# Performance work log

Hardware: AMD Instinct MI355X
Metric: run time of the kernel (lower is better)

## Reference

```python
import jax, jax.numpy as jnp
from jax import lax
import numpy as np

D_STATE = 16
D_CONV = 4
GROUPS = 4
TOKEN = 8


def group_norm(x, w, b, groups, eps=1e-5):
    # x: [B, C, H, W]; torch GroupNorm semantics
    B, C, H, W = x.shape
    xg = x.reshape(B, groups, C // groups, H, W)
    mu = xg.mean(axis=(2, 3, 4), keepdims=True)
    var = ((xg - mu) ** 2).mean(axis=(2, 3, 4), keepdims=True)
    xg = (xg - mu) / jnp.sqrt(var + eps)
    return xg.reshape(B, C, H, W) * w[None, :, None, None] + b[None, :, None, None]


def mamba_fwd(x, in_w, conv_w, conv_b, xproj_w, dt_w, dt_b, A_log, D, out_w):
    # x: [B, L, d_model]. Faithful mamba_ssm Mamba forward (no biases on in/out proj).
    Bsz, L, _ = x.shape
    d_inner = in_w.shape[0] // 2
    dt_rank = dt_w.shape[1]
    xz = x @ in_w.T                                   # [B, L, 2*d_inner]
    xi, z = jnp.split(xz, 2, axis=-1)
    # causal depthwise conv1d (kernel D_CONV) + SiLU
    xc = lax.conv_general_dilated(
        xi.transpose(0, 2, 1), conv_w, window_strides=(1,),
        padding=[(D_CONV - 1, 0)], dimension_numbers=("NCH", "OIH", "NCH"),
        feature_group_count=d_inner)
    xc = jax.nn.silu(xc + conv_b[None, :, None]).transpose(0, 2, 1)  # [B, L, d_inner]
    xdb = xc @ xproj_w.T                               # [B, L, dt_rank + 2*d_state]
    dt, Bm, Cm = jnp.split(xdb, [dt_rank, dt_rank + D_STATE], axis=-1)
    dt = jax.nn.softplus(dt @ dt_w.T + dt_b)           # [B, L, d_inner]
    A = -jnp.exp(A_log)                                # [d_inner, d_state]
    dA = jnp.exp(dt[..., None] * A)                    # [B, L, d_inner, d_state]
    dBx = dt[..., None] * Bm[:, :, None, :] * xc[..., None]

    def step(h, inp):
        dA_t, dBx_t, C_t = inp                         # [B,di,ds],[B,di,ds],[B,ds]
        h = dA_t * h + dBx_t
        y = jnp.einsum('bds,bs->bd', h, C_t)
        return h, y

    h0 = jnp.zeros((Bsz, d_inner, D_STATE), dtype=x.dtype)
    _, ys = lax.scan(step, h0, (dA.transpose(1, 0, 2, 3),
                                dBx.transpose(1, 0, 2, 3),
                                Cm.transpose(1, 0, 2)))
    y = ys.transpose(1, 0, 2) + xc * D                 # skip term D*x
    y = y * jax.nn.silu(z)
    return y @ out_w.T


def setup_inputs() -> dict:
    key = jax.random.key(0)
    ks = iter(jax.random.split(key, 48))

    def rn(shape, s=0.02):
        return jax.random.normal(next(ks), shape, dtype=jnp.float32) * s

    B, C, H, W = 4, 64, 64, 64
    inp = {"x": jax.random.normal(next(ks), (B, C, H, W), dtype=jnp.float32)}

    def mamba_params(prefix, d_model):
        d_inner = 2 * d_model
        dt_rank = -(-d_model // 16)
        inp[prefix + "_in_w"] = rn((2 * d_inner, d_model))
        inp[prefix + "_conv_w"] = rn((d_inner, 1, D_CONV))
        inp[prefix + "_conv_b"] = rn((d_inner,))
        inp[prefix + "_xproj_w"] = rn((dt_rank + 2 * D_STATE, d_inner))
        inp[prefix + "_dt_w"] = rn((d_inner, dt_rank))
        inp[prefix + "_dt_b"] = rn((d_inner,)) + 0.5
        inp[prefix + "_A_log"] = jnp.log(jnp.tile(jnp.arange(1, D_STATE + 1, dtype=jnp.float32), (d_inner, 1)))
        inp[prefix + "_D"] = jnp.ones((d_inner,), jnp.float32)
        inp[prefix + "_out_w"] = rn((d_model, d_inner))

    mamba_params("spa", C)
    mamba_params("spe", -(-C // TOKEN))  # group_channel_num = ceil(64/8) = 8
    inp["spa_gn_w"] = jnp.ones((C,), jnp.float32)
    inp["spa_gn_b"] = jnp.zeros((C,), jnp.float32)
    inp["spe_gn_w"] = jnp.ones((C,), jnp.float32)
    inp["spe_gn_b"] = jnp.zeros((C,), jnp.float32)
    inp["att_w"] = jnp.full((2,), 0.5, jnp.float32)
    return inp


def reference(x,
              spa_in_w, spa_conv_w, spa_conv_b, spa_xproj_w, spa_dt_w, spa_dt_b,
              spa_A_log, spa_D, spa_out_w,
              spe_in_w, spe_conv_w, spe_conv_b, spe_xproj_w, spe_dt_w, spe_dt_b,
              spe_A_log, spe_D, spe_out_w,
              spa_gn_w, spa_gn_b, spe_gn_w, spe_gn_b, att_w):
    B, C, H, W = x.shape
    gcn = -(-C // TOKEN)  # C == TOKEN*gcn here, so no padding path is taken

    # --- SpaMamba: flatten all pixels into one sequence [1, B*H*W, C] ---
    xs = x.transpose(0, 2, 3, 1).reshape(1, -1, C)
    ys = mamba_fwd(xs, spa_in_w, spa_conv_w, spa_conv_b, spa_xproj_w,
                   spa_dt_w, spa_dt_b, spa_A_log, spa_D, spa_out_w)
    ys = ys.reshape(B, H, W, C).transpose(0, 3, 1, 2)
    spa = jax.nn.silu(group_norm(ys, spa_gn_w, spa_gn_b, GROUPS)) + x

    # --- SpeMamba: per-pixel spectral tokens [B*H*W, TOKEN, gcn] ---
    xe = x.transpose(0, 2, 3, 1).reshape(B * H * W, TOKEN, gcn)
    ye = mamba_fwd(xe, spe_in_w, spe_conv_w, spe_conv_b, spe_xproj_w,
                   spe_dt_w, spe_dt_b, spe_A_log, spe_D, spe_out_w)
    ye = ye.reshape(B, H, W, C).transpose(0, 3, 1, 2)
    spe = x + jax.nn.silu(group_norm(ye, spe_gn_w, spe_gn_b, GROUPS))

    w = jax.nn.softmax(att_w)
    return spa * w[0] + spe * w[1] + x
```

## Files before the change

### kernel.cpp

```cpp
#include <hip/hip_runtime.h>

__device__ __forceinline__ float siluf(float x){ return x / (1.f + __expf(-x)); }
__device__ __forceinline__ float softplusf(float x){
    return fmaxf(x, 0.f) + __logf(1.f + __expf(-fabsf(x)));
}
#if __has_builtin(__builtin_amdgcn_exp2f)
__device__ __forceinline__ float fexp2(float x){ return __builtin_amdgcn_exp2f(x); }
#else
__device__ __forceinline__ float fexp2(float x){ return exp2f(x); }
#endif

__global__ void __launch_bounds__(256) k_xpose(const float* __restrict__ x, float* __restrict__ xs){
    __shared__ float t[64][65];
    int blk = blockIdx.x;
    int b = blk >> 6;
    int hw0 = (blk & 63) << 6;
    int tid = threadIdx.x;
    if (blk == 0 && tid < 192) xs[tid] = 0.f;
    const float* xb = x + b*262144 + hw0;
    #pragma unroll
    for (int it = 0; it < 16; ++it){
        int idx = it*256 + tid;
        t[idx>>6][idx&63] = xb[(idx>>6)*4096 + (idx&63)];
    }
    __syncthreads();
    float* xsb = xs + 192 + (size_t)(b*4096 + hw0)*64;
    #pragma unroll
    for (int it = 0; it < 16; ++it){
        int idx = it*256 + tid;
        xsb[(idx>>6)*64 + (idx&63)] = t[idx&63][idx>>6];
    }
}

__global__ void __launch_bounds__(256) k_inproj_conv(const float* __restrict__ xs,
        const float* __restrict__ in_w, const float* __restrict__ cw, const float* __restrict__ cb,
        float* __restrict__ xc, float* __restrict__ zb){
    int tid = threadIdx.x;
    int l0 = blockIdx.x * 8;
    float wr[64];
    const float4* w4 = (const float4*)(in_w + tid*64);
    #pragma unroll
    for (int k = 0; k < 16; ++k){
        float4 v = w4[k];
        wr[4*k]=v.x; wr[4*k+1]=v.y; wr[4*k+2]=v.z; wr[4*k+3]=v.w;
    }
    if (tid < 128){
        float acc[11];
        #pragma unroll
        for (int r = 0; r < 11; ++r) acc[r] = 0.f;
        const float4* xr = ((const float4*)xs) + (size_t)l0*16;
        #pragma unroll
        for (int k = 0; k < 16; ++k){
            #pragma unroll
            for (int r = 0; r < 11; ++r){
                float4 v = xr[r*16 + k];
                acc[r] = fmaf(v.x, wr[4*k],   acc[r]);
                acc[r] = fmaf(v.y, wr[4*k+1], acc[r]);
                acc[r] = fmaf(v.z, wr[4*k+2], acc[r]);
                acc[r] = fmaf(v.w, wr[4*k+3], acc[r]);
            }
        }
        float cw0 = cw[tid*4+0], cw1 = cw[tid*4+1], cw2 = cw[tid*4+2], cw3 = cw[tid*4+3];
        float cbd = cb[tid];
        #pragma unroll
        for (int r = 0; r < 8; ++r){
            float a = fmaf(cw0, acc[r],   cbd);
            a = fmaf(cw1, acc[r+1], a);
            a = fmaf(cw2, acc[r+2], a);
            a = fmaf(cw3, acc[r+3], a);
            xc[(size_t)(l0+r)*128 + tid] = siluf(a);
        }
    } else {
        float acc[8];
        #pragma unroll
        for (int r = 0; r < 8; ++r) acc[r] = 0.f;
        const float4* xr = ((const float4*)(xs + 192)) + (size_t)l0*16;
        #pragma unroll
        for (int k = 0; k < 16; ++k){
            #pragma unroll
            for (int r = 0; r < 8; ++r){
                float4 v = xr[r*16 + k];
                acc[r] = fmaf(v.x, wr[4*k],   acc[r]);
                acc[r] = fmaf(v.y, wr[4*k+1], acc[r]);
                acc[r] = fmaf(v.z, wr[4*k+2], acc[r]);
                acc[r] = fmaf(v.w, wr[4*k+3], acc[r]);
            }
        }
        int dz = tid - 128;
        #pragma unroll
        for (int r = 0; r < 8; ++r) zb[(size_t)(l0+r)*128 + dz] = acc[r];
    }
}

__global__ void __launch_bounds__(256) k_p1_spe(
        const float* __restrict__ xc, const float* __restrict__ xpw, const float* __restrict__ dtw,
        const float* __restrict__ dtb, const float* __restrict__ A_log,
        float* __restrict__ Pb, float* __restrict__ Qb,
        const float* __restrict__ x,
        const float* __restrict__ ein_w, const float* __restrict__ ecw, const float* __restrict__ ecb,
        const float* __restrict__ expw, const float* __restrict__ edtw, const float* __restrict__ edtb,
        const float* __restrict__ eA_log, const float* __restrict__ eDv, const float* __restrict__ eow,
        float* __restrict__ ye, float* __restrict__ sp)
{
    __shared__ float smem[9960];
    const int tid = threadIdx.x;
    if (blockIdx.x < 512){
        float* sxc = smem;
        float* sbm = smem + 4096;
        float* dtr = smem + 4608;
        const int ch = blockIdx.x;
        {
            const float4* src = (const float4*)(xc + (size_t)ch*4096);
            float4* dst = (float4*)sxc;
            #pragma unroll
            for (int u = 0; u < 4; ++u) dst[u*256 + tid] = src[u*256 + tid];
        }
        __syncthreads();
        {
            int j = tid & 63, tg = tid >> 6;
            if (j < 20){
                const float4* w4  = (const float4*)(xpw + j*128);
                const float4* xc4 = (const float4*)sxc + tg*256;
                float acc[8];
                #pragma unroll
                for (int r = 0; r < 8; ++r) acc[r] = 0.f;
                #pragma unroll 8
                for (int k = 0; k < 32; ++k){
                    float4 w = w4[k];
                    #pragma unroll
                    for (int r = 0; r < 8; ++r){
                        float4 v = xc4[r*32 + k];
                        acc[r] = fmaf(v.x, w.x, acc[r]);
                        acc[r] = fmaf(v.y, w.y, acc[r]);
                        acc[r] = fmaf(v.z, w.z, acc[r]);
                        acc[r] = fmaf(v.w, w.w, acc[r]);
                    }
                }
                if (j < 4){
                    #pragma unroll
                    for (int r = 0; r < 8; ++r) dtr[(tg*8+r)*4 + j] = acc[r];
                } else {
                    #pragma unroll
                    for (int r = 0; r < 8; ++r) sbm[(tg*8+r)*16 + (j-4)] = acc[r];
                }
            }
        }
        __syncthreads();
        const int d  = tid & 127;
        const int sh = tid >> 7;
        float A8[8];
        {
            const float4* al4 = (const float4*)(A_log + d*16 + sh*8);
            float4 v0 = al4[0], v1 = al4[1];
            A8[0]=-__expf(v0.x)*1.44269504f; A8[1]=-__expf(v0.y)*1.44269504f;
            A8[2]=-__expf(v0.z)*1.44269504f; A8[3]=-__expf(v0.w)*1.44269504f;
            A8[4]=-__expf(v1.x)*1.44269504f; A8[5]=-__expf(v1.y)*1.44269504f;
            A8[6]=-__expf(v1.z)*1.44269504f; A8[7]=-__expf(v1.w)*1.44269504f;
        }
        float4 dw = *(const float4*)(dtw + d*4);
        float dbd = dtb[d];
        float P[8], Q[8];
        #pragma unroll
        for (int s = 0; s < 8; ++s){ P[s] = 1.f; Q[s] = 0.f; }
        #pragma unroll 4
        for (int i = 0; i < 32; ++i){
            float4 dt4 = *(const float4*)(dtr + i*4);
            float dv = dbd;
            dv = fmaf(dt4.x, dw.x, dv);
            dv = fmaf(dt4.y, dw.y, dv);
            dv = fmaf(dt4.z, dw.z, dv);
            dv = fmaf(dt4.w, dw.w, dv);
            float dt = softplusf(dv);
            float db = dt * sxc[i*128 + d];
            const float4* bmr = (const float4*)(sbm + i*16 + sh*8);
            float4 b0 = bmr[0], b1 = bmr[1];
            float bv[8] = {b0.x,b0.y,b0.z,b0.w,b1.x,b1.y,b1.z,b1.w};
            #pragma unroll
            for (int s = 0; s < 8; ++s){
                float a = fexp2(dt*A8[s]);
                P[s] *= a;
                Q[s] = fmaf(a, Q[s], db*bv[s]);
            }
        }
        float* Pp = Pb + (size_t)ch*2048 + d*16 + sh*8;
        float* Qp = Qb + (size_t)ch*2048 + d*16 + sh*8;
        ((float4*)Pp)[0] = make_float4(P[0],P[1],P[2],P[3]);
        ((float4*)Pp)[1] = make_float4(P[4],P[5],P[6],P[7]);
        ((float4*)Qp)[0] = make_float4(Q[0],Q[1],Q[2],Q[3]);
        ((float4*)Qp)[1] = make_float4(Q[4],Q[5],Q[6],Q[7]);
    } else {
        float* xe  = smem;
        float* xcl = smem + 1088;
        float* bml = smem + 3264;
        float* cml = smem + 5440;
        float* dtl = smem + 7616;
        float* yl  = smem + 7752;
        float* spg = smem + 9928;
        const int pix = tid >> 4;
        const int d   = tid & 15;
        const int eb  = blockIdx.x - 512;
        const int p0  = eb * 16;
        const int b   = p0 >> 12;
        const int hw0 = p0 & 4095;

        const float* xb = x + b*262144 + hw0;
        #pragma unroll
        for (int it = 0; it < 4; ++it){
            int idx = it*256 + tid;
            xe[(idx>>4)*17 + (idx&15)] = xb[(idx>>4)*4096 + (idx&15)];
        }
        __syncthreads();

        float wi[8], wz[8];
        #pragma unroll
        for (int g = 0; g < 8; ++g){ wi[g] = ein_w[d*8+g]; wz[g] = ein_w[(16+d)*8+g]; }
        float xi[8], zz[8];
        #pragma unroll
        for (int t = 0; t < 8; ++t){
            float ai = 0.f, az = 0.f;
            #pragma unroll
            for (int g = 0; g < 8; ++g){
                float v = xe[(t*8+g)*17 + pix];
                ai = fmaf(v, wi[g], ai);
                az = fmaf(v, wz[g], az);
            }
            xi[t] = ai; zz[t] = az;
        }
        float c0 = ecw[d*4+0], c1 = ecw[d*4+1], c2 = ecw[d*4+2], c3 = ecw[d*4+3];
        float cbd = ecb[d];
        float xcr[8];
        #pragma unroll
        for (int t = 0; t < 8; ++t){
            float a = fmaf(c3, xi[t], cbd);
            if (t >= 1) a = fmaf(c2, xi[t-1], a);
            if (t >= 2) a = fmaf(c1, xi[t-2], a);
            if (t >= 3) a = fmaf(c0, xi[t-3], a);
            xcr[t] = siluf(a);
            xcl[(t*16+d)*17 + pix] = xcr[t];
        }
        __syncthreads();

        {
            const float* wr = expw + d*16;
            #pragma unroll
            for (int t = 0; t < 8; ++t){
                float acc = 0.f;
                #pragma unroll
                for (int k = 0; k < 16; ++k) acc = fmaf(xcl[(t*16+k)*17 + pix], wr[k], acc);
                if (d == 0) dtl[t*17 + pix] = acc;
                else bml[(t*16+d-1)*17 + pix] = acc;
            }
        }
        {
            const float* wr = expw + (17+d)*16;
            #pragma unroll
            for (int t = 0; t < 8; ++t){
                float acc = 0.f;
                #pragma unroll
                for (int k = 0; k < 16; ++k) acc = fmaf(xcl[(t*16+k)*17 + pix], wr[k], acc);
                cml[(t*16+d)*17 + pix] = acc;
            }
        }
        if (d == 15){
            const float* wr = expw + 16*16;
            #pragma unroll
            for (int t = 0; t < 8; ++t){
                float acc = 0.f;
                #pragma unroll
                for (int k = 0; k < 16; ++k) acc = fmaf(xcl[(t*16+k)*17 + pix], wr[k], acc);
                bml[(t*16+15)*17 + pix] = acc;
            }
        }
        __syncthreads();

        float A16[16];
        #pragma unroll
        for (int s = 0; s < 16; ++s) A16[s] = -__expf(eA_log[d*16+s]) * 1.44269504f;
        float dwd = edtw[d], dbd = edtb[d], Dd = eDv[d];
        float h[16];
        #pragma unroll
        for (int s = 0; s < 16; ++s) h[s] = 0.f;
        #pragma unroll
        for (int t = 0; t < 8; ++t){
            float dtd = softplusf(fmaf(dtl[t*17 + pix], dwd, dbd));
            float db = dtd * xcr[t];
            float yp = 0.f;
            #pragma unroll
            for (int s = 0; s < 16; ++s){
                float a = fexp2(dtd*A16[s]);
                h[s] = fmaf(a, h[s], db*bml[(t*16+s)*17 + pix]);
                yp = fmaf(h[s], cml[(t*16+s)*17 + pix], yp);
            }
            yl[(t*16+d)*17 + pix] = (yp + xcr[t]*Dd) * siluf(zz[t]);
        }
        __syncthreads();

        int t = d >> 1, m0 = (d & 1)*4;
        float acc[4];
        #pragma unroll
        for (int mm = 0; mm < 4; ++mm){
            const float* wr = eow + (m0+mm)*16;
            float a = 0.f;
            #pragma unroll
            for (int k = 0; k < 16; ++k) a = fmaf(yl[(t*16+k)*17 + pix], wr[k], a);
            acc[mm] = a;
        }
        float4 o; o.x=acc[0]; o.y=acc[1]; o.z=acc[2]; o.w=acc[3];
        *(float4*)(ye + (size_t)(p0+pix)*64 + t*8 + m0) = o;

        float s  = acc[0]+acc[1]+acc[2]+acc[3];
        float ss = acc[0]*acc[0]+acc[1]*acc[1]+acc[2]*acc[2]+acc[3]*acc[3];
        s += __shfl_xor(s,1);  ss += __shfl_xor(ss,1);
        s += __shfl_xor(s,2);  ss += __shfl_xor(ss,2);
        s += __shfl_xor(s,16); ss += __shfl_xor(ss,16);
        s += __shfl_xor(s,32); ss += __shfl_xor(ss,32);
        int lane = tid & 63, wv = tid >> 6;
        if ((lane & 51) == 0){ spg[0*16 + wv*4 + ((lane>>2)&3)] = s; spg[16 + wv*4 + ((lane>>2)&3)] = ss; }
        __syncthreads();
        if (tid < 4){
            int blk = eb & 255;
            float S  = spg[0*16+0*4+tid]+spg[0*16+1*4+tid]+spg[0*16+2*4+tid]+spg[0*16+3*4+tid];
            float SS = spg[16+0*4+tid]+spg[16+1*4+tid]+spg[16+2*4+tid]+spg[16+3*4+tid];
            float* dst = sp + (size_t)(((4 + b)*4 + tid)*512 + blk*2);
            dst[0] = S; dst[1] = SS;
        }
    }
}

__global__ void __launch_bounds__(256) k_scan_p2a(const float* __restrict__ Pb,
        const float* __restrict__ Qb, float* __restrict__ Ps, float* __restrict__ Qs){
    int g = blockIdx.x*256 + threadIdx.x;
    int sup = g >> 11;
    int lane = g & 2047;
    float P = 1.f, Q = 0.f;
    for (int i = 0; i < 32; i += 8){
        float p[8], q[8];
        #pragma unroll
        for (int u = 0; u < 8; ++u){
            p[u] = Pb[(size_t)(sup*32+i+u)*2048 + lane];
            q[u] = Qb[(size_t)(sup*32+i+u)*2048 + lane];
        }
        #pragma unroll
        for (int u = 0; u < 8; ++u){
            P = p[u]*P;
            Q = fmaf(p[u], Q, q[u]);
        }
    }
    Ps[g] = P; Qs[g] = Q;
}

__global__ void __launch_bounds__(256) k_scan_p2c(const float* __restrict__ Pb,
        const float* __restrict__ Qb, const float* __restrict__ Ps,
        const float* __restrict__ Qs, float* __restrict__ Hs){
    int g = blockIdx.x*256 + threadIdx.x;
    int sup = g >> 11;
    int lane = g & 2047;
    float h = 0.f;
    for (int u = 0; u < sup; ++u){
        float p = Ps[u*2048 + lane];
        float q = Qs[u*2048 + lane];
        h = fmaf(p, h, q);
    }
    for (int i = 0; i < 32; i += 8){
        float p[8], q[8];
        #pragma unroll
        for (int u = 0; u < 8; ++u){
            p[u] = Pb[(size_t)(sup*32+i+u)*2048 + lane];
            q[u] = Qb[(size_t)(sup*32+i+u)*2048 + lane];
        }
        #pragma unroll
        for (int u = 0; u < 8; ++u){
            Hs[(size_t)(sup*32+i+u)*2048 + lane] = h;
            h = fmaf(p[u], h, q[u]);
        }
    }
}

__global__ void __launch_bounds__(256) k_scan_p3(const float* __restrict__ xc,
        const float* __restrict__ zb, const float* __restrict__ xpw, const float* __restrict__ dtw,
        const float* __restrict__ dtb, const float* __restrict__ A_log, const float* __restrict__ Dv,
        const float* __restrict__ Hs, const float* __restrict__ ow,
        float* __restrict__ ys, float* __restrict__ sp){
    __shared__ float sxc[32*128];
    __shared__ float ypl[2][32*128];
    __shared__ float sbm[32*16];
    __shared__ float scm[32*16];
    __shared__ __align__(16) float dtr[32][4];
    __shared__ float pgs[2][2][4];
    const int tid = threadIdx.x;
    const int ch = blockIdx.x;
    {
        const float4* src = (const float4*)(xc + (size_t)ch*4096);
        float4* dst = (float4*)sxc;
        #pragma unroll
        for (int u = 0; u < 4; ++u) dst[u*256 + tid] = src[u*256 + tid];
    }
    __syncthreads();
    {
        int j = tid & 63, tg = tid >> 6;
        if (j < 36){
            const float4* w4  = (const float4*)(xpw + j*128);
            const float4* xc4 = (const float4*)sxc + tg*256;
            float acc[8];
            #pragma unroll
            for (int r = 0; r < 8; ++r) acc[r] = 0.f;
            #pragma unroll 8
            for (int k = 0; k < 32; ++k){
                float4 w = w4[k];
                #pragma unroll
                for (int r = 0; r < 8; ++r){
                    float4 v = xc4[r*32 + k];
                    acc[r] = fmaf(v.x, w.x, acc[r]);
                    acc[r] = fmaf(v.y, w.y, acc[r]);
                    acc[r] = fmaf(v.z, w.z, acc[r]);
                    acc[r] = fmaf(v.w, w.w, acc[r]);
                }
            }
            if (j < 4){
                #pragma unroll
                for (int r = 0; r < 8; ++r) dtr[tg*8+r][j] = acc[r];
            } else if (j < 20){
                #pragma unroll
                for (int r = 0; r < 8; ++r) sbm[(tg*8+r)*16 + (j-4)] = acc[r];
            } else {
                #pragma unroll
                for (int r = 0; r < 8; ++r) scm[(tg*8+r)*16 + (j-20)] = acc[r];
            }
        }
    }
    __syncthreads();
    const int d  = tid & 127;
    const int sh = tid >> 7;
    float A8[8], h[8];
    {
        const float4* al4 = (const float4*)(A_log + d*16 + sh*8);
        float4 v0 = al4[0], v1 = al4[1];
        A8[0]=-__expf(v0.x)*1.44269504f; A8[1]=-__expf(v0.y)*1.44269504f;
        A8[2]=-__expf(v0.z)*1.44269504f; A8[3]=-__expf(v0.w)*1.44269504f;
        A8[4]=-__expf(v1.x)*1.44269504f; A8[5]=-__expf(v1.y)*1.44269504f;
        A8[6]=-__expf(v1.z)*1.44269504f; A8[7]=-__expf(v1.w)*1.44269504f;
        const float4* h4 = (const float4*)(Hs + (size_t)ch*2048 + d*16 + sh*8);
        float4 h0 = h4[0], h1 = h4[1];
        h[0]=h0.x; h[1]=h0.y; h[2]=h0.z; h[3]=h0.w;
        h[4]=h1.x; h[5]=h1.y; h[6]=h1.z; h[7]=h1.w;
    }
    float4 dw = *(const float4*)(dtw + d*4);
    float dbd = dtb[d];
    #pragma unroll 4
    for (int i = 0; i < 32; ++i){
        float4 dt4 = *(const float4*)dtr[i];
        float dv = dbd;
        dv = fmaf(dt4.x, dw.x, dv);
        dv = fmaf(dt4.y, dw.y, dv);
        dv = fmaf(dt4.z, dw.z, dv);
        dv = fmaf(dt4.w, dw.w, dv);
        float dt = softplusf(dv);
        float db = dt * sxc[i*128 + d];
        const float4* bmr = (const float4*)(sbm + i*16 + sh*8);
        const float4* cmr = (const float4*)(scm + i*16 + sh*8);
        float4 b0 = bmr[0], b1 = bmr[1];
        float4 c0 = cmr[0], c1 = cmr[1];
        float bv[8] = {b0.x,b0.y,b0.z,b0.w,b1.x,b1.y,b1.z,b1.w};
        float cv[8] = {c0.x,c0.y,c0.z,c0.w,c1.x,c1.y,c1.z,c1.w};
        float yp = 0.f;
        #pragma unroll
        for (int s = 0; s < 8; ++s){
            float a = fexp2(dt*A8[s]);
            h[s] = fmaf(a, h[s], db*bv[s]);
            yp = fmaf(h[s], cv[s], yp);
        }
        ypl[sh][i*128 + d] = yp;
    }
    __syncthreads();
    #pragma unroll
    for (int it = 0; it < 16; ++it){
        int idx = it*256 + tid;
        float yp = ypl[0][idx] + ypl[1][idx];
        float xcd = sxc[idx];
        float zv = zb[(size_t)ch*4096 + idx];
        ypl[0][idx] = (yp + xcd*Dv[idx & 127]) * siluf(zv);
    }
    __syncthreads();
    {
        int c  = tid & 63;
        int kh = (tid >> 6) & 1;
        int rg = tid >> 7;
        float wr[64];
        const float4* w4o = (const float4*)(ow + c*128 + kh*64);
        #pragma unroll
        for (int k = 0; k < 16; ++k){
            float4 v = w4o[k];
            wr[4*k]=v.x; wr[4*k+1]=v.y; wr[4*k+2]=v.z; wr[4*k+3]=v.w;
        }
        float acc[16];
        #pragma unroll
        for (int r = 0; r < 16; ++r) acc[r] = 0.f;
        const float4* y4 = (const float4*)(ypl[0] + rg*16*128 + kh*64);
        #pragma unroll
        for (int k = 0; k < 16; ++k){
            #pragma unroll
            for (int r = 0; r < 16; ++r){
                float4 v = y4[r*32 + k];
                acc[r] = fmaf(v.x, wr[4*k],   acc[r]);
                acc[r] = fmaf(v.y, wr[4*k+1], acc[r]);
                acc[r] = fmaf(v.z, wr[4*k+2], acc[r]);
                acc[r] = fmaf(v.w, wr[4*k+3], acc[r]);
            }
        }
        float* part = ypl[1];
        if (kh == 1){
            #pragma unroll
            for (int r = 0; r < 16; ++r) part[(rg*16+r)*64 + c] = acc[r];
        }
        __syncthreads();
        if (kh == 0){
            float s = 0.f, ss = 0.f;
            #pragma unroll
            for (int r = 0; r < 16; ++r){
                float v = acc[r] + part[(rg*16+r)*64 + c];
                ys[(size_t)(ch*32 + rg*16 + r)*64 + c] = v;
                s += v; ss += v*v;
            }
            s += __shfl_xor(s,1); ss += __shfl_xor(ss,1);
            s += __shfl_xor(s,2); ss += __shfl_xor(ss,2);
            s += __shfl_xor(s,4); ss += __shfl_xor(ss,4);
            s += __shfl_xor(s,8); ss += __shfl_xor(ss,8);
            if ((c & 15) == 0){ pgs[0][rg][c>>4] = s; pgs[1][rg][c>>4] = ss; }
        }
        __syncthreads();
        if (tid < 4){
            int b = ch >> 7, blk = ch & 127;
            float S  = pgs[0][0][tid] + pgs[0][1][tid];
            float SS = pgs[1][0][tid] + pgs[1][1][tid];
            float* dst = sp + (size_t)((b*4 + tid)*512 + blk*2);
            dst[0] = S; dst[1] = SS;
        }
    }
}

__global__ void __launch_bounds__(256) k_final(const float* __restrict__ x,
        const float* __restrict__ ys, const float* __restrict__ ye,
        const float* __restrict__ sp,
        const float* __restrict__ gsw, const float* __restrict__ gsb,
        const float* __restrict__ gew, const float* __restrict__ geb,
        const float* __restrict__ attw, float* __restrict__ out){
    __shared__ float st[16];
    __shared__ float tys[32][65];
    __shared__ float tye[32][65];
    int tid = threadIdx.x;
    int b   = blockIdx.x >> 7;
    int hw0 = (blockIdx.x & 127) << 5;
    {
        int combo = tid >> 5;
        int j = tid & 31;
        int t = combo >> 2, g = combo & 3;
        float s = 0.f, ss = 0.f;
        if (t == 0){
            const float4* bp = (const float4*)(sp + (size_t)(b*4 + g)*512 + j*8);
            #pragma unroll
            for (int k = 0; k < 2; ++k){ float4 v = bp[k]; s += v.x+v.z; ss += v.y+v.w; }
        } else {
            const float4* bp = (const float4*)(sp + (size_t)((4+b)*4 + g)*512 + j*16);
            #pragma unroll
            for (int k = 0; k < 4; ++k){ float4 v = bp[k]; s += v.x+v.z; ss += v.y+v.w; }
        }
        s += __shfl_xor(s,1);  ss += __shfl_xor(ss,1);
        s += __shfl_xor(s,2);  ss += __shfl_xor(ss,2);
        s += __shfl_xor(s,4);  ss += __shfl_xor(ss,4);
        s += __shfl_xor(s,8);  ss += __shfl_xor(ss,8);
        s += __shfl_xor(s,16); ss += __shfl_xor(ss,16);
        if (j == 0){
            float m = s * (1.f/65536.f);
            float v = ss * (1.f/65536.f) - m*m;
            st[combo*2]   = m;
            st[combo*2+1] = rsqrtf(v + 1e-5f);
        }
    }
    const float* ysb = ys + ((size_t)(b*4096 + hw0))*64;
    const float* yeb = ye + ((size_t)(b*4096 + hw0))*64;
    #pragma unroll
    for (int it = 0; it < 8; ++it){
        int idx = it*256 + tid;
        tys[idx>>6][idx&63] = ysb[idx];
        tye[idx>>6][idx&63] = yeb[idx];
    }
    __syncthreads();
    float a0 = attw[0], a1 = attw[1];
    float mx = fmaxf(a0, a1);
    float e0 = __expf(a0-mx), e1 = __expf(a1-mx);
    float inv = 1.f/(e0+e1);
    float w0 = e0*inv, w1 = e1*inv;
    #pragma unroll
    for (int it = 0; it < 8; ++it){
        int idx = it*256 + tid;
        int c = idx >> 5, hwi = idx & 31;
        int g = c >> 4;
        size_t gx = ((size_t)(b*64 + c))*4096 + hw0 + hwi;
        float xv = x[gx];
        float ns = (tys[hwi][c] - st[g*2])     * st[g*2+1]     * gsw[c] + gsb[c];
        float ne = (tye[hwi][c] - st[8+g*2])   * st[8+g*2+1]   * gew[c] + geb[c];
        out[gx] = w0*(siluf(ns)+xv) + w1*(xv+siluf(ne)) + xv;
    }
}

#define OFF_XS 0u
#define OFF_XC 1048832u
#define OFF_Z  3145984u
#define OFF_PB 5243136u
#define OFF_QB 6291712u
#define OFF_HS 7340288u
#define OFF_YE 8388864u
#define OFF_PS 9437440u
#define OFF_QS 9470208u
#define OFF_SP 9502976u

extern "C" void kernel_launch(void* const* d_in, const int* in_sizes, int n_in,
                              void* d_out, int out_size, void* d_ws, size_t ws_size,
                              hipStream_t stream) {
    const float* x           = (const float*)d_in[0];
    const float* spa_in_w    = (const float*)d_in[1];
    const float* spa_conv_w  = (const float*)d_in[2];
    const float* spa_conv_b  = (const float*)d_in[3];
    const float* spa_xproj_w = (const float*)d_in[4];
    const float* spa_dt_w    = (const float*)d_in[5];
    const float* spa_dt_b    = (const float*)d_in[6];
    const float* spa_A_log   = (const float*)d_in[7];
    const float* spa_D       = (const float*)d_in[8];
    const float* spa_out_w   = (const float*)d_in[9];
    const float* spe_in_w    = (const float*)d_in[10];
    const float* spe_conv_w  = (const float*)d_in[11];
    const float* spe_conv_b  = (const float*)d_in[12];
    const float* spe_xproj_w = (const float*)d_in[13];
    const float* spe_dt_w    = (const float*)d_in[14];
    const float* spe_dt_b    = (const float*)d_in[15];
    const float* spe_A_log   = (const float*)d_in[16];
    const float* spe_D       = (const float*)d_in[17];
    const float* spe_out_w   = (const float*)d_in[18];
    const float* spa_gn_w    = (const float*)d_in[19];
    const float* spa_gn_b    = (const float*)d_in[20];
    const float* spe_gn_w    = (const float*)d_in[21];
    const float* spe_gn_b    = (const float*)d_in[22];
    const float* att_w       = (const float*)d_in[23];

    float* ws  = (float*)d_ws;
    float* xs  = ws + OFF_XS;
    float* xc  = ws + OFF_XC;
    float* zb  = ws + OFF_Z;
    float* Pb  = ws + OFF_PB;
    float* Qb  = ws + OFF_QB;
    float* Hs  = ws + OFF_HS;
    float* Ps  = ws + OFF_PS;
    float* Qs  = ws + OFF_QS;
    float* sp  = ws + OFF_SP;
    float* ysb = ws + OFF_XS;
    float* yeb = ws + OFF_YE;
    float* out = (float*)d_out;

    k_xpose      <<<256,  256, 0, stream>>>(x, xs);
    k_inproj_conv<<<2048, 256, 0, stream>>>(xs, spa_in_w, spa_conv_w, spa_conv_b, xc, zb);
    k_p1_spe     <<<1536, 256, 0, stream>>>(xc, spa_xproj_w, spa_dt_w, spa_dt_b, spa_A_log,
                                            Pb, Qb,
                                            x, spe_in_w, spe_conv_w, spe_conv_b, spe_xproj_w,
                                            spe_dt_w, spe_dt_b, spe_A_log, spe_D, spe_out_w,
                                            yeb, sp);
    k_scan_p2a   <<<128,  256, 0, stream>>>(Pb, Qb, Ps, Qs);
    k_scan_p2c   <<<128,  256, 0, stream>>>(Pb, Qb, Ps, Qs, Hs);
    k_scan_p3    <<<512,  256, 0, stream>>>(xc, zb, spa_xproj_w, spa_dt_w, spa_dt_b,
                                            spa_A_log, spa_D, Hs, spa_out_w, ysb, sp);
    k_final      <<<512,  256, 0, stream>>>(x, ysb, yeb, sp, spa_gn_w, spa_gn_b,
                                            spe_gn_w, spe_gn_b, att_w, out);
}
```

Before: 120.2 us.

## Restructure spectral-Mamba shared-memory layout for vectorized reads and reorder block roles

The spectral branch of the fused kernel now stores its intermediates pixel-major in shared memory, with padded strides, so per-thread rows can be read as float4 instead of scalar strided loads. The x_proj matmul is repartitioned so each thread pair computes the 16 B or 16 C outputs for one (pixel, token) row, which replaces the per-d loops and the serialized d==15 pass. Shared memory shrinks from 9960 to 8800 floats, and the spectral blocks now take the low block indices while the spatial chunk blocks move to the high ones. Risks are new bank conflicts on the padded strides and higher register pressure from the 16-wide temporary arrays.

```diff
diff --git a/kernel.cpp b/kernel.cpp
--- a/kernel.cpp
+++ b/kernel.cpp
@@ -92,6 +92,11 @@
     }
 }
 
+#define XE_  0
+#define XCL_ 1216
+#define BCL_ 3904
+#define DTV_ 8640
+#define SPG_ 8768
 __global__ void __launch_bounds__(256) k_p1_spe(
         const float* __restrict__ xc, const float* __restrict__ xpw, const float* __restrict__ dtw,
         const float* __restrict__ dtb, const float* __restrict__ A_log,
@@ -102,13 +107,13 @@
         const float* __restrict__ eA_log, const float* __restrict__ eDv, const float* __restrict__ eow,
         float* __restrict__ ye, float* __restrict__ sp)
 {
-    __shared__ float smem[9960];
+    __shared__ float smem[8800];
     const int tid = threadIdx.x;
-    if (blockIdx.x < 512){
+    if (blockIdx.x >= 1024){
         float* sxc = smem;
         float* sbm = smem + 4096;
         float* dtr = smem + 4608;
-        const int ch = blockIdx.x;
+        const int ch = blockIdx.x - 1024;
         {
             const float4* src = (const float4*)(xc + (size_t)ch*4096);
             float4* dst = (float4*)sxc;
@@ -189,16 +194,9 @@
         ((float4*)Qp)[0] = make_float4(Q[0],Q[1],Q[2],Q[3]);
         ((float4*)Qp)[1] = make_float4(Q[4],Q[5],Q[6],Q[7]);
     } else {
-        float* xe  = smem;
-        float* xcl = smem + 1088;
-        float* bml = smem + 3264;
-        float* cml = smem + 5440;
-        float* dtl = smem + 7616;
-        float* yl  = smem + 7752;
-        float* spg = smem + 9928;
         const int pix = tid >> 4;
         const int d   = tid & 15;
-        const int eb  = blockIdx.x - 512;
+        const int eb  = blockIdx.x;
         const int p0  = eb * 16;
         const int b   = p0 >> 12;
         const int hw0 = p0 & 4095;
@@ -207,7 +205,7 @@
         #pragma unroll
         for (int it = 0; it < 4; ++it){
             int idx = it*256 + tid;
-            xe[(idx>>4)*17 + (idx&15)] = xb[(idx>>4)*4096 + (idx&15)];
+            smem[XE_ + (idx&15)*76 + (idx>>4)] = xb[(idx>>4)*4096 + (idx&15)];
         }
         __syncthreads();
 
@@ -215,16 +213,20 @@
         #pragma unroll
         for (int g = 0; g < 8; ++g){ wi[g] = ein_w[d*8+g]; wz[g] = ein_w[(16+d)*8+g]; }
         float xi[8], zz[8];
-        #pragma unroll
-        for (int t = 0; t < 8; ++t){
-            float ai = 0.f, az = 0.f;
-            #pragma unroll
-            for (int g = 0; g < 8; ++g){
-                float v = xe[(t*8+g)*17 + pix];
-                ai = fmaf(v, wi[g], ai);
-                az = fmaf(v, wz[g], az);
-            }
-            xi[t] = ai; zz[t] = az;
+        {
+            const float4* xe4 = (const float4*)(smem + XE_ + pix*76);
+            #pragma unroll
+            for (int t = 0; t < 8; ++t){
+                float4 a = xe4[t*2], bq = xe4[t*2+1];
+                float xv8[8] = {a.x,a.y,a.z,a.w,bq.x,bq.y,bq.z,bq.w};
+                float ai = 0.f, az = 0.f;
+                #pragma unroll
+                for (int g = 0; g < 8; ++g){
+                    ai = fmaf(xv8[g], wi[g], ai);
+                    az = fmaf(xv8[g], wz[g], az);
+                }
+                xi[t] = ai; zz[t] = az;
+            }
         }
         float c0 = ecw[d*4+0], c1 = ecw[d*4+1], c2 = ecw[d*4+2], c3 = ecw[d*4+3];
         float cbd = ecb[d];
@@ -236,40 +238,36 @@
             if (t >= 2) a = fmaf(c1, xi[t-2], a);
             if (t >= 3) a = fmaf(c0, xi[t-3], a);
             xcr[t] = siluf(a);
-            xcl[(t*16+d)*17 + pix] = xcr[t];
+            smem[XCL_ + pix*168 + t*20 + d] = xcr[t];
         }
         __syncthreads();
 
         {
-            const float* wr = expw + d*16;
-            #pragma unroll
-            for (int t = 0; t < 8; ++t){
-                float acc = 0.f;
+            const int row = tid >> 1;
+            const int jh  = tid & 1;
+            const int px2 = row >> 3;
+            const int t2  = row & 7;
+            const float4* xr = (const float4*)(smem + XCL_ + px2*168 + t2*20);
+            float4 r0 = xr[0], r1 = xr[1], r2 = xr[2], r3 = xr[3];
+            float xv[16] = {r0.x,r0.y,r0.z,r0.w, r1.x,r1.y,r1.z,r1.w,
+                            r2.x,r2.y,r2.z,r2.w, r3.x,r3.y,r3.z,r3.w};
+            float accd = 0.f;
+            #pragma unroll
+            for (int k = 0; k < 16; ++k) accd = fmaf(xv[k], expw[k], accd);
+            const float* wbase = expw + (1 + jh*16)*16;
+            float outv[16];
+            #pragma unroll
+            for (int s = 0; s < 16; ++s){
+                const float* wr = wbase + s*16;
+                float a = 0.f;
                 #pragma unroll
-                for (int k = 0; k < 16; ++k) acc = fmaf(xcl[(t*16+k)*17 + pix], wr[k], acc);
-                if (d == 0) dtl[t*17 + pix] = acc;
-                else bml[(t*16+d-1)*17 + pix] = acc;
-            }
-        }
-        {
-            const float* wr = expw + (17+d)*16;
-            #pragma unroll
-            for (int t = 0; t < 8; ++t){
-                float acc = 0.f;
-                #pragma unroll
-                for (int k = 0; k < 16; ++k) acc = fmaf(xcl[(t*16+k)*17 + pix], wr[k], acc);
-                cml[(t*16+d)*17 + pix] = acc;
-            }
-        }
-        if (d == 15){
-            const float* wr = expw + 16*16;
-            #pragma unroll
-            for (int t = 0; t < 8; ++t){
-                float acc = 0.f;
-                #pragma unroll
-                for (int k = 0; k < 16; ++k) acc = fmaf(xcl[(t*16+k)*17 + pix], wr[k], acc);
-                bml[(t*16+15)*17 + pix] = acc;
-            }
+                for (int k = 0; k < 16; ++k) a = fmaf(xv[k], wr[k], a);
+                outv[s] = a;
+            }
+            float* dstb = smem + BCL_ + px2*296 + t2*36 + jh*16;
+            #pragma unroll
+            for (int s = 0; s < 16; ++s) dstb[s] = outv[s];
+            if (jh == 0) smem[DTV_ + px2*8 + t2] = accd;
         }
         __syncthreads();
 
@@ -282,31 +280,42 @@
         for (int s = 0; s < 16; ++s) h[s] = 0.f;
         #pragma unroll
         for (int t = 0; t < 8; ++t){
-            float dtd = softplusf(fmaf(dtl[t*17 + pix], dwd, dbd));
+            float dtd = softplusf(fmaf(smem[DTV_ + pix*8 + t], dwd, dbd));
             float db = dtd * xcr[t];
+            const float4* bc4 = (const float4*)(smem + BCL_ + pix*296 + t*36);
+            float4 b0 = bc4[0], b1 = bc4[1], b2 = bc4[2], b3 = bc4[3];
+            float4 cc0 = bc4[4], cc1 = bc4[5], cc2 = bc4[6], cc3 = bc4[7];
+            float bv[16] = {b0.x,b0.y,b0.z,b0.w, b1.x,b1.y,b1.z,b1.w,
+                            b2.x,b2.y,b2.z,b2.w, b3.x,b3.y,b3.z,b3.w};
+            float cv[16] = {cc0.x,cc0.y,cc0.z,cc0.w, cc1.x,cc1.y,cc1.z,cc1.w,
+                            cc2.x,cc2.y,cc2.z,cc2.w, cc3.x,cc3.y,cc3.z,cc3.w};
             float yp = 0.f;
             #pragma unroll
             for (int s = 0; s < 16; ++s){
                 float a = fexp2(dtd*A16[s]);
-                h[s] = fmaf(a, h[s], db*bml[(t*16+s)*17 + pix]);
-                yp = fmaf(h[s], cml[(t*16+s)*17 + pix], yp);
-            }
-            yl[(t*16+d)*17 + pix] = (yp + xcr[t]*Dd) * siluf(zz[t]);
-        }
-        __syncthreads();
-
-        int t = d >> 1, m0 = (d & 1)*4;
+                h[s] = fmaf(a, h[s], db*bv[s]);
+                yp = fmaf(h[s], cv[s], yp);
+            }
+            smem[pix*168 + t*20 + d] = (yp + xcr[t]*Dd) * siluf(zz[t]);
+        }
+        __syncthreads();
+
+        int tt = d >> 1, m0 = (d & 1)*4;
+        const float4* y4 = (const float4*)(smem + pix*168 + tt*20);
+        float4 y0 = y4[0], y1 = y4[1], y2 = y4[2], y3 = y4[3];
+        float ylr[16] = {y0.x,y0.y,y0.z,y0.w, y1.x,y1.y,y1.z,y1.w,
+                         y2.x,y2.y,y2.z,y2.w, y3.x,y3.y,y3.z,y3.w};
         float acc[4];
         #pragma unroll
         for (int mm = 0; mm < 4; ++mm){
             const float* wr = eow + (m0+mm)*16;
             float a = 0.f;
             #pragma unroll
-            for (int k = 0; k < 16; ++k) a = fmaf(yl[(t*16+k)*17 + pix], wr[k], a);
+            for (int k = 0; k < 16; ++k) a = fmaf(ylr[k], wr[k], a);
             acc[mm] = a;
         }
         float4 o; o.x=acc[0]; o.y=acc[1]; o.z=acc[2]; o.w=acc[3];
-        *(float4*)(ye + (size_t)(p0+pix)*64 + t*8 + m0) = o;
+        *(float4*)(ye + (size_t)(p0+pix)*64 + tt*8 + m0) = o;
 
         float s  = acc[0]+acc[1]+acc[2]+acc[3];
         float ss = acc[0]*acc[0]+acc[1]*acc[1]+acc[2]*acc[2]+acc[3]*acc[3];
@@ -315,12 +324,12 @@
         s += __shfl_xor(s,16); ss += __shfl_xor(ss,16);
         s += __shfl_xor(s,32); ss += __shfl_xor(ss,32);
         int lane = tid & 63, wv = tid >> 6;
-        if ((lane & 51) == 0){ spg[0*16 + wv*4 + ((lane>>2)&3)] = s; spg[16 + wv*4 + ((lane>>2)&3)] = ss; }
+        if ((lane & 51) == 0){ smem[SPG_ + wv*4 + ((lane>>2)&3)] = s; smem[SPG_ + 16 + wv*4 + ((lane>>2)&3)] = ss; }
         __syncthreads();
         if (tid < 4){
             int blk = eb & 255;
-            float S  = spg[0*16+0*4+tid]+spg[0*16+1*4+tid]+spg[0*16+2*4+tid]+spg[0*16+3*4+tid];
-            float SS = spg[16+0*4+tid]+spg[16+1*4+tid]+spg[16+2*4+tid]+spg[16+3*4+tid];
+            float S  = smem[SPG_+0*4+tid]+smem[SPG_+1*4+tid]+smem[SPG_+2*4+tid]+smem[SPG_+3*4+tid];
+            float SS = smem[SPG_+16+0*4+tid]+smem[SPG_+16+1*4+tid]+smem[SPG_+16+2*4+tid]+smem[SPG_+16+3*4+tid];
             float* dst = sp + (size_t)(((4 + b)*4 + tid)*512 + blk*2);
             dst[0] = S; dst[1] = SS;
         }
```

New measurement: 120.2 us. No clear change (-0.0%).
